# Kernel tuning notes

Hardware: AMD Instinct MI355X
Metric: run time of the kernel (lower is better)

## Reference

```python
import jax, jax.numpy as jnp
import numpy as np

EPS = 1e-12  # F.normalize eps

def _unfold3(x):
    # x: [B,C,H,W] -> [B, C*9, H*W], matching F.unfold(kernel=3, padding=1)
    B, C, H, W = x.shape
    xp = jnp.pad(x, ((0, 0), (0, 0), (1, 1), (1, 1)))
    pats = jnp.stack([xp[:, :, i:i + H, j:j + W]
                      for i in range(3) for j in range(3)], axis=2)  # [B,C,9,H,W]
    return pats.reshape(B, C * 9, H * W)

def _fold3(t, H, W):
    # inverse of _unfold3 with overlap-add, matching F.fold(kernel=3, padding=1)
    B, CK, L = t.shape
    C = CK // 9
    t = t.reshape(B, C, 3, 3, H, W)
    out = jnp.zeros((B, C, H + 2, W + 2), t.dtype)
    for i in range(3):
        for j in range(3):
            out = out.at[:, :, i:i + H, j:j + W].add(t[:, :, i, j])
    return out[:, :, 1:1 + H, 1:1 + W]

def setup_inputs() -> dict:
    key = jax.random.key(0)
    kV, kK, kQ = jax.random.split(key, 3)
    B, C, H, W = 4, 64, 64, 64
    return {
        'V': jax.random.normal(kV, (B, C, H, W), dtype=jnp.float32),
        'K': jax.random.normal(kK, (B, C, H, W), dtype=jnp.float32),
        'Q': jax.random.normal(kQ, (B, C, H, W), dtype=jnp.float32),
    }

def reference(V, K, Q):
    B, C, H, W = Q.shape
    Qu = _unfold3(Q)  # [B, C9, L]
    Ku = _unfold3(K)  # [B, C9, L]
    # F.normalize along the feature (C*9) axis for both K (after permute dim=2) and Q (dim=1)
    Kn = Ku / jnp.maximum(jnp.linalg.norm(Ku, axis=1, keepdims=True), EPS)
    Qn = Qu / jnp.maximum(jnp.linalg.norm(Qu, axis=1, keepdims=True), EPS)
    # R[b,k,q] = <Kn[b,:,k], Qn[b,:,q]>  -> [B, L, L]
    R = jnp.einsum('bfk,bfq->bkq', Kn, Qn)
    S = jnp.max(R, axis=1)        # [B, L]
    arg = jnp.argmax(R, axis=1)   # [B, L] best key patch per query position
    Vu = _unfold3(V)              # [B, C9, L]
    idx = jnp.broadcast_to(arg[:, None, :], Vu.shape)
    T_unfold = jnp.take_along_axis(Vu, idx, axis=2)  # gather along patch dim
    T = _fold3(T_unfold, H, W) / 9.0                 # [B, C, H, W]
    S = S.reshape(B, 1, H, W)
    return (S, T)
```

## Files before the change

### kernel.cpp

```cpp
#include <hip/hip_runtime.h>
#include <math.h>

#define HW 4096

typedef short bf16x8 __attribute__((ext_vector_type(8)));
typedef float floatx4 __attribute__((ext_vector_type(4)));
typedef unsigned short u16x8 __attribute__((ext_vector_type(8)));

__device__ __forceinline__ unsigned short f2bf_rne(float x) {
    unsigned int u = __float_as_uint(x);
    unsigned int r = (u + 0x7FFFu + ((u >> 16) & 1u)) >> 16;
    return (unsigned short)r;
}
__device__ __forceinline__ float bf2f(unsigned short h) {
    return __uint_as_float(((unsigned int)h) << 16);
}

__device__ __forceinline__ void gload_lds16(const void* gptr, void* lptr) {
    auto g = (const __attribute__((address_space(1))) unsigned int*)(unsigned long long)(gptr);
    auto l = (__attribute__((address_space(3))) unsigned int*)(unsigned int)(unsigned long long)(lptr);
    __builtin_amdgcn_global_load_lds(g, l, 16, 0, 0);
}

__global__ __launch_bounds__(256)
void prep_kernel(const float* __restrict__ Q, const float* __restrict__ K,
                 const float* __restrict__ V,
                 unsigned short* __restrict__ Aq, unsigned short* __restrict__ Bq,
                 float* __restrict__ VT,
                 float* __restrict__ pix2q, float* __restrict__ pix2k) {
    __shared__ float sT[64][65];
    const int tid = threadIdx.x;
    const int p0 = blockIdx.x * 64;
    const int b = blockIdx.y;
    const int which = blockIdx.z;
    const float* __restrict__ src = (which == 0) ? Q : ((which == 1) ? K : V);

#pragma unroll
    for (int it = 0; it < 16; ++it) {
        int idx = it * 256 + tid;
        int c = idx >> 6, x = idx & 63;
        sT[c][x] = src[((size_t)b * 64 + c) * HW + p0 + x];
    }
    __syncthreads();
    const int pp = tid >> 2, qt = tid & 3;

    if (which == 2) {
        float* dst = VT + ((size_t)b * 4096 + p0 + pp) * 64 + qt * 16;
#pragma unroll
        for (int j = 0; j < 4; ++j) {
            float4 v = make_float4(sT[qt * 16 + 4 * j + 0][pp], sT[qt * 16 + 4 * j + 1][pp],
                                   sT[qt * 16 + 4 * j + 2][pp], sT[qt * 16 + 4 * j + 3][pp]);
            *(float4*)(dst + 4 * j) = v;
        }
        return;
    }

    const int isK = which;
    unsigned short* __restrict__ dst = isK ? Bq : Aq;
    float* __restrict__ pix2 = isK ? pix2k : pix2q;
    const size_t base = ((size_t)b * 4096 + p0 + pp) * 192;
    {
        float sq = 0.f;
        u16x8 hv[2], lv[2];
#pragma unroll
        for (int g = 0; g < 2; ++g)
#pragma unroll
            for (int j = 0; j < 8; ++j) {
                int c = qt * 16 + g * 8 + j;
                float x = sT[c][pp];
                sq = fmaf(x, x, sq);
                unsigned short h = f2bf_rne(x);
                hv[g][j] = h;
                lv[g][j] = f2bf_rne(x - bf2f(h));
            }
        sq += __shfl_xor(sq, 1, 64);
        sq += __shfl_xor(sq, 2, 64);
        if (qt == 0) pix2[(b << 12) + p0 + pp] = sq;
#pragma unroll
        for (int g = 0; g < 2; ++g) {
            int co = qt * 16 + g * 8;
            *(u16x8*)(dst + base + co)                     = hv[g];
            *(u16x8*)(dst + base + (isK ? 64 : 128) + co)  = lv[g];
        }
    }
}

#define WAITV(n_) asm volatile("s_waitcnt vmcnt(" #n_ ")" ::: "memory")
#define PBAR(n_) do { WAITV(n_); __builtin_amdgcn_s_barrier(); \
                      asm volatile("" ::: "memory"); } while (0)
#define SB do { __builtin_amdgcn_s_barrier(); asm volatile("" ::: "memory"); } while (0)

#define ISSUE_A(c_, sg_, slot_) \
    gload_lds16(agb + (size_t)((c_) * 64 + rr) * 384 + (sg_) * 128 + G16, \
                smem + (slot_) * 8192 + t16)
#define ISSUE_B(c_, sg_, slot_) \
    gload_lds16(bgb + (size_t)((c_) * 64 + rr) * 384 + (sg_) * 128 + G16, \
                smemB + (slot_) * 8192 + t16)

#define GISS_A(c_, sg_, slot_) do { \
    uint4 v_ = make_uint4(0u, 0u, 0u, 0u); \
    if ((unsigned)(arow + (c_) * 64 + rr) < 4096u) \
        v_ = *(const uint4*)(agb + (ptrdiff_t)((c_) * 64 + rr) * 384 + (sg_) * 128 + G16); \
    *(uint4*)(smem + (slot_) * 8192 + t16) = v_; \
} while (0)
#define GISS_B(c_, sg_, slot_) do { \
    uint4 v_ = make_uint4(0u, 0u, 0u, 0u); \
    if ((unsigned)(brow + (c_) * 64 + rr) < 4096u) \
        v_ = *(const uint4*)(bgb + (ptrdiff_t)((c_) * 64 + rr) * 384 + (sg_) * 128 + G16); \
    *(uint4*)(smemB + (slot_) * 8192 + t16) = v_; \
} while (0)

#define MM8(af_, bf_) do { \
    _Pragma("unroll") \
    for (int mt_ = 0; mt_ < 4; ++mt_) \
        _Pragma("unroll") \
        for (int nt_ = 0; nt_ < 2; ++nt_) \
            acc[mt_][nt_] = __builtin_amdgcn_mfma_f32_16x16x32_bf16( \
                (af_)[mt_], (bf_)[nt_], acc[mt_][nt_], 0, 0, 0); \
} while (0)

#define DY_MEGA(dy_) do { \
    const char* AhS_ = smem + ahS[wm + (dy_)] * 8192 + rowB; \
    const char* AlS_ = smem + alS[wm + (dy_)] * 8192 + rowB; \
    const char* BhS_ = smemB + bhS[wnC + (dy_)] * 8192 + rowBB; \
    const char* BlS_ = smemB + blS[wnC + (dy_)] * 8192 + rowBB; \
    _Pragma("unroll") \
    for (int kk = 0; kk < 2; ++kk) { \
        const int pk_ = kk ? posK1 : posK0; \
        bf16x8 afc[4], bfc[2], bl2[2], al4[4]; \
        _Pragma("unroll") \
        for (int mt = 0; mt < 4; ++mt) \
            afc[mt] = *(const bf16x8*)(AhS_ + mt * 2048 + pk_); \
        _Pragma("unroll") \
        for (int nt = 0; nt < 2; ++nt) \
            bfc[nt] = *(const bf16x8*)(BhS_ + nt * 2048 + pk_); \
        _Pragma("unroll") \
        for (int nt = 0; nt < 2; ++nt) \
            bl2[nt] = *(const bf16x8*)(BlS_ + nt * 2048 + pk_); \
        _Pragma("unroll") \
        for (int mt = 0; mt < 4; ++mt) \
            al4[mt] = *(const bf16x8*)(AlS_ + mt * 2048 + pk_); \
        __builtin_amdgcn_s_setprio(1); \
        MM8(afc, bfc); \
        MM8(afc, bl2); \
        MM8(al4, bfc); \
        __builtin_amdgcn_s_setprio(0); \
    } \
} while (0)

__global__ __launch_bounds__(512, 4)
void gemm_fused_kernel(const unsigned short* __restrict__ Aq, const unsigned short* __restrict__ Bq,
                       const float* __restrict__ pix2k,
                       float* __restrict__ part_val, int* __restrict__ part_arg) {
    __shared__ __align__(16) char smem[81920];
    char* const smemB = smem + 40960;
    const int tid = threadIdx.x;
    const int lane = tid & 63, wid = tid >> 6;
    const int m15 = lane & 15, quad = lane >> 4;
    const int wm = wid & 1;
    const int wn2 = wid >> 1;
    const int wnC = wn2 >> 1, wnF = wn2 & 1;
    const int ahS[4] = {0, 1, 4, 2};
    const int alS[4] = {2, 3, 0, 3};
    const int bhS[4] = {0, 1, 4, 2};
    const int blS[4] = {2, 3, 0, 3};
    const int f = blockIdx.x + (blockIdx.y << 5);
    const int o = ((f & 7) << 7) + (f >> 3);
    const int kt = o & 31, qt = o >> 5;
    const int k0 = kt << 7;
    const int q0 = qt << 7;
    const int b = blockIdx.z;
    const int arow = q0 - 64, brow = k0 - 64;
    const char* agb = (const char*)(Aq + (size_t)b * 4096 * 192) + (ptrdiff_t)arow * 384;
    const char* bgb = (const char*)(Bq + (size_t)b * 4096 * 192) + (ptrdiff_t)brow * 384;
    const bool aInt = (q0 >= 64) && (q0 <= 4096 - 192);
    const bool bInt = (k0 >= 64) && (k0 <= 4096 - 192);

    const int rr = tid >> 3;
    const int G16 = ((tid & 7) ^ (rr & 7)) * 16;
    const int t16 = tid * 16;
    const int rowB = m15 * 128;
    const int rowBB = (wnF * 32 + m15) * 128;
    const int posK0 = (quad ^ (m15 & 7)) * 16;
    const int posK1 = ((4 + quad) ^ (m15 & 7)) * 16;

    float pk9[9];
    if (tid < 128) {
        int k = k0 + tid;
        int py = k >> 6, px = k & 63;
#pragma unroll
        for (int t = 0; t < 9; ++t) {
            int yy = py + t / 3 - 1, xx = px + t % 3 - 1;
            pk9[t] = ((unsigned)yy < 64u && (unsigned)xx < 64u)
                   ? pix2k[(b << 12) + (yy << 6) + xx] : 0.f;
        }
    } else {
#pragma unroll
        for (int t = 0; t < 9; ++t) pk9[t] = 0.f;
    }

    floatx4 acc[4][2];
#pragma unroll
    for (int i = 0; i < 4; ++i)
#pragma unroll
        for (int j = 0; j < 2; ++j) acc[i][j] = (floatx4)0.f;

    if (aInt && bInt) {
        ISSUE_A(0, 0, 0); ISSUE_A(1, 0, 1); ISSUE_B(0, 0, 0); ISSUE_B(1, 0, 1);
        ISSUE_A(0, 2, 2); ISSUE_A(1, 2, 3); ISSUE_B(0, 1, 2); ISSUE_B(1, 1, 3);
        ISSUE_A(2, 0, 4); ISSUE_B(2, 0, 4);
        PBAR(2);
        DY_MEGA(0);
        SB;
        ISSUE_A(2, 2, 0);
        ISSUE_B(2, 1, 0);
        ISSUE_A(3, 0, 2);
        ISSUE_B(3, 0, 2);
        PBAR(2);
        DY_MEGA(1);
        SB;
        ISSUE_A(3, 2, 3);
        ISSUE_B(3, 1, 3);
        PBAR(0);
        DY_MEGA(2);
    } else {
        GISS_A(0, 0, 0); GISS_A(1, 0, 1); GISS_B(0, 0, 0); GISS_B(1, 0, 1);
        GISS_A(0, 2, 2); GISS_A(1, 2, 3); GISS_B(0, 1, 2); GISS_B(1, 1, 3);
        GISS_A(2, 0, 4); GISS_B(2, 0, 4);
        __syncthreads();
        DY_MEGA(0);
        __syncthreads();
        GISS_A(2, 2, 0); GISS_B(2, 1, 0); GISS_A(3, 0, 2); GISS_B(3, 0, 2);
        __syncthreads();
        DY_MEGA(1);
        __syncthreads();
        GISS_A(3, 2, 3); GISS_B(3, 1, 3);
        __syncthreads();
        DY_MEGA(2);
    }
    __syncthreads();

    float* Csh = (float*)smem;
    float* bvs = (float*)(smem + 34816);
    int*   bas = (int*)(smem + 36864);
    float* Lrnk = (float*)(smem + 38912);
    if (tid < 128) {
        float sk = 0.f;
#pragma unroll
        for (int t = 0; t < 9; ++t) sk += pk9[t];
        Lrnk[tid] = 1.f / fmaxf(sqrtf(sk), 1e-12f);
    }
    const int q_l = tid & 63;
    const int qr = tid >> 6;
    const int c0 = qr * 16;
    const float4 zero4 = make_float4(0.f, 0.f, 0.f, 0.f);

#pragma unroll
    for (int h = 0; h < 2; ++h) {
        if (h) __syncthreads();
        if (wm == h) {
#pragma unroll
            for (int mt = 0; mt < 4; ++mt)
#pragma unroll
                for (int nt = 0; nt < 2; ++nt)
#pragma unroll
                    for (int j = 0; j < 4; ++j)
                        Csh[(mt * 16 + quad * 4 + j) * 133 + (wn2 << 5) + nt * 16 + m15] =
                            acc[mt][nt][j];
        }
        __syncthreads();

        const bool qm = q_l > 0;
        const bool qp = q_l < 63;
        const float* rC = Csh + q_l * 133;
        const float* rM = Csh + (q_l - 1) * 133;
        const float* rP = Csh + (q_l + 1) * 133;
        float4 prevm = (qm && c0 > 0) ? *(const float4*)&rM[c0 - 4] : zero4;
        float4 rpj   = qp ? *(const float4*)&rP[c0] : zero4;
        float bv = -INFINITY;
        int ba = 0;
#pragma unroll
        for (int j = 0; j < 4; ++j) {
            int c = c0 + 4 * j;
            float4 cen = *(const float4*)&rC[c];
            float4 rm4 = qm ? *(const float4*)&rM[c] : zero4;
            float4 rp1 = (qp && (c + 4) < 128) ? *(const float4*)&rP[c + 4] : zero4;
            float4 o4;
            o4.x = cen.x + (((c & 63) != 0) ? prevm.w : 0.f) + rpj.y;
            o4.y = cen.y + rm4.x + rpj.z;
            o4.z = cen.z + rm4.y + rpj.w;
            o4.w = cen.w + rm4.z + ((((c + 3) & 63) != 63) ? rp1.x : 0.f);
            float4 rk = *(const float4*)&Lrnk[c];
            float v0 = o4.x * rk.x; if (v0 > bv) { bv = v0; ba = k0 + c + 0; }
            float v1 = o4.y * rk.y; if (v1 > bv) { bv = v1; ba = k0 + c + 1; }
            float v2 = o4.z * rk.z; if (v2 > bv) { bv = v2; ba = k0 + c + 2; }
            float v3 = o4.w * rk.w; if (v3 > bv) { bv = v3; ba = k0 + c + 3; }
            prevm = rm4;
            rpj = rp1;
        }
        bvs[(qr << 6) + q_l] = bv;
        bas[(qr << 6) + q_l] = ba;
        __syncthreads();
        if (tid < 64) {
            float v = bvs[tid];
            int a = bas[tid];
#pragma unroll
            for (int s = 1; s < 8; ++s) {
                float v2 = bvs[(s << 6) + tid];
                if (v2 > v) { v = v2; a = bas[(s << 6) + tid]; }
            }
            int q = q0 + h * 64 + tid;
            part_val[(((b << 5) + kt) << 12) + q] = v;
            part_arg[(((b << 5) + kt) << 12) + q] = a;
        }
    }
}

__global__ __launch_bounds__(256)
void argcombine_kernel(const float* __restrict__ part_val, const int* __restrict__ part_arg,
                       const float* __restrict__ pix2q,
                       float* __restrict__ S_out, int* __restrict__ argF) {
    __shared__ float rv[4][64];
    __shared__ int ra[4][64];
    const int tid = threadIdx.x;
    const int qi = tid & 63, sg = tid >> 6;
    const int q = blockIdx.x * 64 + qi;
    const int b = blockIdx.y;
    const int base = (b << 17) + q;
    float bv = -INFINITY; int ba = 0;
#pragma unroll
    for (int i = 0; i < 8; ++i) {
        int s = sg * 8 + i;
        float v = part_val[base + (s << 12)];
        int aa = part_arg[base + (s << 12)];
        if (v > bv) { bv = v; ba = aa; }
    }
    rv[sg][qi] = bv; ra[sg][qi] = ba;
    __syncthreads();
    if (tid < 64) {
        float v = rv[0][tid]; int a = ra[0][tid];
#pragma unroll
        for (int s = 1; s < 4; ++s) {
            float v2 = rv[s][tid];
            if (v2 > v) { v = v2; a = ra[s][tid]; }
        }
        int py = blockIdx.x, px = tid;
        float sq = 0.f;
        for (int dy = -1; dy <= 1; ++dy)
            for (int dx = -1; dx <= 1; ++dx) {
                int y2 = py + dy, x2 = px + dx;
                if ((unsigned)y2 < 64u && (unsigned)x2 < 64u)
                    sq += pix2q[(b << 12) + (y2 << 6) + x2];
            }
        int idx = (b << 12) + (py << 6) + px;
        S_out[idx] = v * (1.f / fmaxf(sqrtf(sq), 1e-12f));
        argF[idx] = a;
    }
}

__global__ __launch_bounds__(256)
void gatherT_kernel(const float* __restrict__ VT, const int* __restrict__ argF,
                    float* __restrict__ T_out) {
    __shared__ int sArg[192];
    const int y = blockIdx.x, b = blockIdx.y, cg = blockIdx.z;
    const int tid = threadIdx.x;
    if (tid < 192) {
        int r = tid >> 6, x = tid & 63;
        int yy = y - 1 + r;
        sArg[tid] = ((unsigned)yy < 64u) ? argF[(b << 12) + (yy << 6) + x] : 0;
    }
    __syncthreads();

    const int x = tid >> 2, cq = tid & 3;
    const float* Vb = VT + (size_t)b * 4096 * 64 + cg * 16 + cq * 4;
    float ax = 0.f, ay = 0.f, az = 0.f, aw = 0.f;
#pragma unroll
    for (int t = 0; t < 9; ++t) {
        int dy = t / 3 - 1, dx = t % 3 - 1;
        int qy = y - dy, qx = x - dx;
        if ((unsigned)qy < 64u && (unsigned)qx < 64u) {
            int a = sArg[(1 - dy) * 64 + qx];
            int sy = (a >> 6) + dy, sx = (a & 63) + dx;
            if ((unsigned)sy < 64u && (unsigned)sx < 64u) {
                float4 v = *(const float4*)(Vb + (size_t)((sy << 6) + sx) * 64);
                ax += v.x; ay += v.y; az += v.z; aw += v.w;
            }
        }
    }
    float* Tb = T_out + ((size_t)b * 64 + cg * 16 + cq * 4) * HW + (y << 6) + x;
    Tb[0]          = ax * (1.f / 9.f);
    Tb[HW]         = ay * (1.f / 9.f);
    Tb[2 * HW]     = az * (1.f / 9.f);
    Tb[3 * HW]     = aw * (1.f / 9.f);
}

extern "C" void kernel_launch(void* const* d_in, const int* in_sizes, int n_in,
                              void* d_out, int out_size, void* d_ws, size_t ws_size,
                              hipStream_t stream) {
    const float* V = (const float*)d_in[0];
    const float* K = (const float*)d_in[1];
    const float* Q = (const float*)d_in[2];
    float* S_out = (float*)d_out;
    float* T_out = S_out + 4 * HW;

    char* ws = (char*)d_ws;
    float* pix2q = (float*)(ws + 0);
    float* pix2k = (float*)(ws + 65536);
    float* part_val = (float*)(ws + 262144);
    int*   argF  = (int*)(ws + 4456448);
    int*   part_arg = (int*)(ws + 8650752);
    float* VT    = (float*)(ws + 10747904);
    unsigned short* Aq = (unsigned short*)(ws + 17039360);
    unsigned short* Bq = (unsigned short*)(ws + 23330816);

    prep_kernel<<<dim3(64, 4, 3), 256, 0, stream>>>(Q, K, V, Aq, Bq, VT, pix2q, pix2k);
    gemm_fused_kernel<<<dim3(32, 32, 4), 512, 0, stream>>>(Aq, Bq, pix2k, part_val, part_arg);
    argcombine_kernel<<<dim3(64, 4), 256, 0, stream>>>(part_val, part_arg, pix2q, S_out, argF);
    gatherT_kernel<<<dim3(64, 4, 4), 256, 0, stream>>>(VT, argF, T_out);
}
```

Measured before the change: 186.1 us.

## Halve GEMM block to 4 waves, each computing a 64x64 tile

The fused correlation GEMM kernel now runs 256 threads (4 waves) per block instead of 512. Each wave computes 4x4 MFMA tiles instead of 4x2, and each thread issues two LDS-direct loads per stage. The epilogue argmax scan covers 32 columns per thread, with a 4-way final reduction. This raises per-wave reuse of A fragments and cuts LDS fragment traffic per MFMA, at the cost of more accumulator registers and less wave-level parallelism per block.

```diff
diff --git a/kernel.cpp b/kernel.cpp
--- a/kernel.cpp
+++ b/kernel.cpp
@@ -90,31 +90,43 @@
                       asm volatile("" ::: "memory"); } while (0)
 #define SB do { __builtin_amdgcn_s_barrier(); asm volatile("" ::: "memory"); } while (0)
 
-#define ISSUE_A(c_, sg_, slot_) \
-    gload_lds16(agb + (size_t)((c_) * 64 + rr) * 384 + (sg_) * 128 + G16, \
-                smem + (slot_) * 8192 + t16)
-#define ISSUE_B(c_, sg_, slot_) \
-    gload_lds16(bgb + (size_t)((c_) * 64 + rr) * 384 + (sg_) * 128 + G16, \
-                smemB + (slot_) * 8192 + t16)
+#define ISSUE_A(c_, sg_, slot_) do { \
+    const char* g_ = agb + (size_t)((c_) * 64) * 384 + (sg_) * 128; \
+    gload_lds16(g_ + g0off, smem + (slot_) * 8192 + l0off); \
+    gload_lds16(g_ + g1off, smem + (slot_) * 8192 + l1off); \
+} while (0)
+#define ISSUE_B(c_, sg_, slot_) do { \
+    const char* g_ = bgb + (size_t)((c_) * 64) * 384 + (sg_) * 128; \
+    gload_lds16(g_ + g0off, smemB + (slot_) * 8192 + l0off); \
+    gload_lds16(g_ + g1off, smemB + (slot_) * 8192 + l1off); \
+} while (0)
 
 #define GISS_A(c_, sg_, slot_) do { \
-    uint4 v_ = make_uint4(0u, 0u, 0u, 0u); \
-    if ((unsigned)(arow + (c_) * 64 + rr) < 4096u) \
-        v_ = *(const uint4*)(agb + (ptrdiff_t)((c_) * 64 + rr) * 384 + (sg_) * 128 + G16); \
-    *(uint4*)(smem + (slot_) * 8192 + t16) = v_; \
+    const char* g_ = agb + (ptrdiff_t)((c_) * 64) * 384 + (sg_) * 128; \
+    uint4 v0_ = make_uint4(0u, 0u, 0u, 0u), v1_ = v0_; \
+    if ((unsigned)(arow + (c_) * 64 + rr0) < 4096u) \
+        v0_ = *(const uint4*)(g_ + g0off); \
+    if ((unsigned)(arow + (c_) * 64 + rr1) < 4096u) \
+        v1_ = *(const uint4*)(g_ + g1off); \
+    *(uint4*)(smem + (slot_) * 8192 + l0off) = v0_; \
+    *(uint4*)(smem + (slot_) * 8192 + l1off) = v1_; \
 } while (0)
 #define GISS_B(c_, sg_, slot_) do { \
-    uint4 v_ = make_uint4(0u, 0u, 0u, 0u); \
-    if ((unsigned)(brow + (c_) * 64 + rr) < 4096u) \
-        v_ = *(const uint4*)(bgb + (ptrdiff_t)((c_) * 64 + rr) * 384 + (sg_) * 128 + G16); \
-    *(uint4*)(smemB + (slot_) * 8192 + t16) = v_; \
-} while (0)
-
-#define MM8(af_, bf_) do { \
+    const char* g_ = bgb + (ptrdiff_t)((c_) * 64) * 384 + (sg_) * 128; \
+    uint4 v0_ = make_uint4(0u, 0u, 0u, 0u), v1_ = v0_; \
+    if ((unsigned)(brow + (c_) * 64 + rr0) < 4096u) \
+        v0_ = *(const uint4*)(g_ + g0off); \
+    if ((unsigned)(brow + (c_) * 64 + rr1) < 4096u) \
+        v1_ = *(const uint4*)(g_ + g1off); \
+    *(uint4*)(smemB + (slot_) * 8192 + l0off) = v0_; \
+    *(uint4*)(smemB + (slot_) * 8192 + l1off) = v1_; \
+} while (0)
+
+#define MM16(af_, bf_) do { \
     _Pragma("unroll") \
     for (int mt_ = 0; mt_ < 4; ++mt_) \
         _Pragma("unroll") \
-        for (int nt_ = 0; nt_ < 2; ++nt_) \
+        for (int nt_ = 0; nt_ < 4; ++nt_) \
             acc[mt_][nt_] = __builtin_amdgcn_mfma_f32_16x16x32_bf16( \
                 (af_)[mt_], (bf_)[nt_], acc[mt_][nt_], 0, 0, 0); \
 } while (0)
@@ -122,33 +134,33 @@
 #define DY_MEGA(dy_) do { \
     const char* AhS_ = smem + ahS[wm + (dy_)] * 8192 + rowB; \
     const char* AlS_ = smem + alS[wm + (dy_)] * 8192 + rowB; \
-    const char* BhS_ = smemB + bhS[wnC + (dy_)] * 8192 + rowBB; \
-    const char* BlS_ = smemB + blS[wnC + (dy_)] * 8192 + rowBB; \
+    const char* BhS_ = smemB + bhS[wn + (dy_)] * 8192 + rowB; \
+    const char* BlS_ = smemB + blS[wn + (dy_)] * 8192 + rowB; \
     _Pragma("unroll") \
     for (int kk = 0; kk < 2; ++kk) { \
         const int pk_ = kk ? posK1 : posK0; \
-        bf16x8 afc[4], bfc[2], bl2[2], al4[4]; \
+        bf16x8 afc[4], bh4[4], bl4[4], al4[4]; \
         _Pragma("unroll") \
         for (int mt = 0; mt < 4; ++mt) \
             afc[mt] = *(const bf16x8*)(AhS_ + mt * 2048 + pk_); \
         _Pragma("unroll") \
-        for (int nt = 0; nt < 2; ++nt) \
-            bfc[nt] = *(const bf16x8*)(BhS_ + nt * 2048 + pk_); \
+        for (int nt = 0; nt < 4; ++nt) \
+            bh4[nt] = *(const bf16x8*)(BhS_ + nt * 2048 + pk_); \
         _Pragma("unroll") \
-        for (int nt = 0; nt < 2; ++nt) \
-            bl2[nt] = *(const bf16x8*)(BlS_ + nt * 2048 + pk_); \
+        for (int nt = 0; nt < 4; ++nt) \
+            bl4[nt] = *(const bf16x8*)(BlS_ + nt * 2048 + pk_); \
         _Pragma("unroll") \
         for (int mt = 0; mt < 4; ++mt) \
             al4[mt] = *(const bf16x8*)(AlS_ + mt * 2048 + pk_); \
         __builtin_amdgcn_s_setprio(1); \
-        MM8(afc, bfc); \
-        MM8(afc, bl2); \
-        MM8(al4, bfc); \
+        MM16(afc, bh4); \
+        MM16(afc, bl4); \
+        MM16(al4, bh4); \
         __builtin_amdgcn_s_setprio(0); \
     } \
 } while (0)
 
-__global__ __launch_bounds__(512, 4)
+__global__ __launch_bounds__(256, 2)
 void gemm_fused_kernel(const unsigned short* __restrict__ Aq, const unsigned short* __restrict__ Bq,
                        const float* __restrict__ pix2k,
                        float* __restrict__ part_val, int* __restrict__ part_arg) {
@@ -157,9 +169,7 @@
     const int tid = threadIdx.x;
     const int lane = tid & 63, wid = tid >> 6;
     const int m15 = lane & 15, quad = lane >> 4;
-    const int wm = wid & 1;
-    const int wn2 = wid >> 1;
-    const int wnC = wn2 >> 1, wnF = wn2 & 1;
+    const int wm = wid & 1, wn = wid >> 1;
     const int ahS[4] = {0, 1, 4, 2};
     const int alS[4] = {2, 3, 0, 3};
     const int bhS[4] = {0, 1, 4, 2};
@@ -176,11 +186,13 @@
     const bool aInt = (q0 >= 64) && (q0 <= 4096 - 192);
     const bool bInt = (k0 >= 64) && (k0 <= 4096 - 192);
 
-    const int rr = tid >> 3;
-    const int G16 = ((tid & 7) ^ (rr & 7)) * 16;
-    const int t16 = tid * 16;
+    const int rr0 = tid >> 3, ps = tid & 7;
+    const int g0off = rr0 * 384 + (ps ^ (rr0 & 7)) * 16;
+    const int l0off = tid * 16;
+    const int rr1 = (256 + tid) >> 3;
+    const int g1off = rr1 * 384 + (ps ^ (rr1 & 7)) * 16;
+    const int l1off = (256 + tid) * 16;
     const int rowB = m15 * 128;
-    const int rowBB = (wnF * 32 + m15) * 128;
     const int posK0 = (quad ^ (m15 & 7)) * 16;
     const int posK1 = ((4 + quad) ^ (m15 & 7)) * 16;
 
@@ -199,24 +211,24 @@
         for (int t = 0; t < 9; ++t) pk9[t] = 0.f;
     }
 
-    floatx4 acc[4][2];
+    floatx4 acc[4][4];
 #pragma unroll
     for (int i = 0; i < 4; ++i)
 #pragma unroll
-        for (int j = 0; j < 2; ++j) acc[i][j] = (floatx4)0.f;
+        for (int j = 0; j < 4; ++j) acc[i][j] = (floatx4)0.f;
 
     if (aInt && bInt) {
         ISSUE_A(0, 0, 0); ISSUE_A(1, 0, 1); ISSUE_B(0, 0, 0); ISSUE_B(1, 0, 1);
         ISSUE_A(0, 2, 2); ISSUE_A(1, 2, 3); ISSUE_B(0, 1, 2); ISSUE_B(1, 1, 3);
         ISSUE_A(2, 0, 4); ISSUE_B(2, 0, 4);
-        PBAR(2);
+        PBAR(4);
         DY_MEGA(0);
         SB;
         ISSUE_A(2, 2, 0);
         ISSUE_B(2, 1, 0);
         ISSUE_A(3, 0, 2);
         ISSUE_B(3, 0, 2);
-        PBAR(2);
+        PBAR(4);
         DY_MEGA(1);
         SB;
         ISSUE_A(3, 2, 3);
@@ -242,8 +254,8 @@
 
     float* Csh = (float*)smem;
     float* bvs = (float*)(smem + 34816);
-    int*   bas = (int*)(smem + 36864);
-    float* Lrnk = (float*)(smem + 38912);
+    int*   bas = (int*)(smem + 35840);
+    float* Lrnk = (float*)(smem + 36864);
     if (tid < 128) {
         float sk = 0.f;
 #pragma unroll
@@ -252,7 +264,7 @@
     }
     const int q_l = tid & 63;
     const int qr = tid >> 6;
-    const int c0 = qr * 16;
+    const int c0 = qr * 32;
     const float4 zero4 = make_float4(0.f, 0.f, 0.f, 0.f);
 
 #pragma unroll
@@ -262,10 +274,10 @@
 #pragma unroll
             for (int mt = 0; mt < 4; ++mt)
 #pragma unroll
-                for (int nt = 0; nt < 2; ++nt)
+                for (int nt = 0; nt < 4; ++nt)
 #pragma unroll
                     for (int j = 0; j < 4; ++j)
-                        Csh[(mt * 16 + quad * 4 + j) * 133 + (wn2 << 5) + nt * 16 + m15] =
+                        Csh[(mt * 16 + quad * 4 + j) * 133 + wn * 64 + nt * 16 + m15] =
                             acc[mt][nt][j];
         }
         __syncthreads();
@@ -280,7 +292,7 @@
         float bv = -INFINITY;
         int ba = 0;
 #pragma unroll
-        for (int j = 0; j < 4; ++j) {
+        for (int j = 0; j < 8; ++j) {
             int c = c0 + 4 * j;
             float4 cen = *(const float4*)&rC[c];
             float4 rm4 = qm ? *(const float4*)&rM[c] : zero4;
@@ -305,7 +317,7 @@
             float v = bvs[tid];
             int a = bas[tid];
 #pragma unroll
-            for (int s = 1; s < 8; ++s) {
+            for (int s = 1; s < 4; ++s) {
                 float v2 = bvs[(s << 6) + tid];
                 if (v2 > v) { v = v2; a = bas[(s << 6) + tid]; }
             }
@@ -414,7 +426,7 @@
     unsigned short* Bq = (unsigned short*)(ws + 23330816);
 
     prep_kernel<<<dim3(64, 4, 3), 256, 0, stream>>>(Q, K, V, Aq, Bq, VT, pix2q, pix2k);
-    gemm_fused_kernel<<<dim3(32, 32, 4), 512, 0, stream>>>(Aq, Bq, pix2k, part_val, part_arg);
+    gemm_fused_kernel<<<dim3(32, 32, 4), 256, 0, stream>>>(Aq, Bq, pix2k, part_val, part_arg);
     argcombine_kernel<<<dim3(64, 4), 256, 0, stream>>>(part_val, part_arg, pix2q, S_out, argF);
     gatherT_kernel<<<dim3(64, 4, 4), 256, 0, stream>>>(VT, argF, T_out);
 }
```

Result: no change. 186.0 us (-0.1%).
